# Optimization experiments

Measured on AMD Instinct MI355X. Metric: run time of the kernel, lower is better.

## Reference

```python
import jax, jax.numpy as jnp
import numpy as np

N = 50000
EH = 500000
ES = 250000
D_IN = 128
D_HID = 128
N_CLS = 47


def _mean_agg(feat, src, dst, n):
    # gather src features, scatter-mean onto dst (DGL copy_u + mean)
    msg = feat[src]                                   # [E, d]
    s = jax.ops.segment_sum(msg, dst, num_segments=n)  # [N, d]
    cnt = jax.ops.segment_sum(jnp.ones((src.shape[0],), feat.dtype), dst, num_segments=n)
    return s / jnp.maximum(cnt, 1.0)[:, None]


def _sage_cv_layer(H, HBar, W, b, hs, hd, ss, sd):
    hbar_new = _mean_agg(HBar, hs, hd, N)             # history etype
    hdelta_new = _mean_agg(H - HBar, ss, sd, N)       # sampled etype
    h_neigh = hbar_new + hdelta_new
    z = jnp.concatenate([H, h_neigh], axis=1)         # [N, 2*d_in]
    return jax.nn.relu(z @ W.T + b)


def setup_inputs() -> dict:
    key = jax.random.key(0)
    ks = jax.random.split(key, 16)
    gain = float(np.sqrt(2.0))  # calculate_gain('relu')

    def xavier(k, shape):
        fan_out, fan_in = shape
        a = gain * np.sqrt(6.0 / (fan_in + fan_out))
        return jax.random.uniform(k, shape, jnp.float32, -a, a)

    return {
        "x": jax.random.normal(ks[0], (N, D_IN), jnp.float32),
        "hbar0": jax.random.normal(ks[1], (N, D_IN), jnp.float32),
        "hbar1": jax.random.normal(ks[2], (N, D_HID), jnp.float32),
        "W0": xavier(ks[3], (D_HID, 2 * D_IN)),
        "b0": jnp.zeros((D_HID,), jnp.float32),
        "W1": xavier(ks[4], (N_CLS, 2 * D_HID)),
        "b1": jnp.zeros((N_CLS,), jnp.float32),
        "hist_src0": jax.random.randint(ks[5], (EH,), 0, N),
        "hist_dst0": jax.random.randint(ks[6], (EH,), 0, N),
        "samp_src0": jax.random.randint(ks[7], (ES,), 0, N),
        "samp_dst0": jax.random.randint(ks[8], (ES,), 0, N),
        "hist_src1": jax.random.randint(ks[9], (EH,), 0, N),
        "hist_dst1": jax.random.randint(ks[10], (EH,), 0, N),
        "samp_src1": jax.random.randint(ks[11], (ES,), 0, N),
        "samp_dst1": jax.random.randint(ks[12], (ES,), 0, N),
    }


def reference(x, hbar0, hbar1, W0, b0, W1, b1,
              hist_src0, hist_dst0, samp_src0, samp_dst0,
              hist_src1, hist_dst1, samp_src1, samp_dst1):
    h = _sage_cv_layer(x, hbar0, W0, b0, hist_src0, hist_dst0, samp_src0, samp_dst0)
    h = _sage_cv_layer(h, hbar1, W1, b1, hist_src1, hist_dst1, samp_src1, samp_dst1)
    return h  # [N, n_classes]
```

## Files before the change

kernel.cpp:

```cpp
#include <hip/hip_runtime.h>

#define D_FEAT 128
#define K_DIM  256
#define EPB 4096

typedef __attribute__((ext_vector_type(8))) short bf16x8;
typedef __attribute__((ext_vector_type(4))) float f32x4;

__device__ __forceinline__ unsigned short f2b(float f) {
    union { float f; unsigned u; } cv; cv.f = f;
    return (unsigned short)((cv.u + 0x7fffu + ((cv.u >> 16) & 1u)) >> 16);
}

__device__ __forceinline__ unsigned pack2(float lo, float hi) {
    return (unsigned)f2b(lo) | ((unsigned)f2b(hi) << 16);
}

__device__ __forceinline__ uint4 pack8(float4 a, float4 b) {
    return make_uint4(pack2(a.x, a.y), pack2(a.z, a.w), pack2(b.x, b.y), pack2(b.z, b.w));
}

__device__ __forceinline__ void addu4(float* a, uint4 v) {
    union { unsigned u; float f; } c;
    c.u = v.x << 16;         a[0] += c.f;
    c.u = v.x & 0xffff0000u; a[1] += c.f;
    c.u = v.y << 16;         a[2] += c.f;
    c.u = v.y & 0xffff0000u; a[3] += c.f;
    c.u = v.z << 16;         a[4] += c.f;
    c.u = v.z & 0xffff0000u; a[5] += c.f;
    c.u = v.w << 16;         a[6] += c.f;
    c.u = v.w & 0xffff0000u; a[7] += c.f;
}

__device__ __forceinline__ long yoff(int y, int EH, int ES) {
    return (long)((y + 1) >> 1) * EH + (long)(y >> 1) * ES;
}


__global__ __launch_bounds__(256)
void histB(const int* __restrict__ hd0, const int* __restrict__ sd0,
           const int* __restrict__ hd1, const int* __restrict__ sd1,
           int EH, int ES, int* __restrict__ bucketCnt, int nb2) {
    int y = blockIdx.y;
    const int* d = (y == 0) ? hd0 : (y == 1) ? sd0 : (y == 2) ? hd1 : sd1;
    int E = (y & 1) ? ES : EH;
    __shared__ int cnt[256];
    int t = threadIdx.x;
    cnt[t] = 0;
    __syncthreads();
    int i0 = blockIdx.x * EPB;
    #pragma unroll
    for (int j = 0; j < 16; ++j) {
        int i = i0 + j * 256 + t;
        if (i < E) atomicAdd(&cnt[d[i] >> 8], 1);
    }
    __syncthreads();
    if (t < nb2 && cnt[t] > 0) atomicAdd(&bucketCnt[y * nb2 + t], cnt[t]);
}

__global__ __launch_bounds__(64)
void scanBuckets(const int* __restrict__ bucketCnt, int* __restrict__ rpBucket,
                 int* __restrict__ bcur, int nb2) {
    int t = threadIdx.x;
    if (t < 4) {
        int run = 0;
        for (int i = 0; i < nb2; ++i) {
            rpBucket[t * (nb2 + 1) + i] = run;
            bcur[t * nb2 + i] = run;
            run += bucketCnt[t * nb2 + i];
        }
        rpBucket[t * (nb2 + 1) + nb2] = run;
    }
}

__global__ __launch_bounds__(256)
void binA(const int* __restrict__ hs0, const int* __restrict__ hd0,
          const int* __restrict__ ss0, const int* __restrict__ sd0,
          const int* __restrict__ hs1, const int* __restrict__ hd1,
          const int* __restrict__ ss1, const int* __restrict__ sd1,
          int EH, int ES, int* __restrict__ bcur, unsigned* __restrict__ recs,
          int nb2) {
    int y = blockIdx.y;
    const int* src = (y == 0) ? hs0 : (y == 1) ? ss0 : (y == 2) ? hs1 : ss1;
    const int* dst = (y == 0) ? hd0 : (y == 1) ? sd0 : (y == 2) ? hd1 : sd1;
    int E = (y & 1) ? ES : EH;
    unsigned* rb = recs + yoff(y, EH, ES);

    __shared__ int cnt[256];
    int t = threadIdx.x;
    cnt[t] = 0;
    __syncthreads();
    int i0 = blockIdx.x * EPB;
    #pragma unroll
    for (int j = 0; j < 16; ++j) {
        int i = i0 + j * 256 + t;
        if (i < E) atomicAdd(&cnt[dst[i] >> 8], 1);
    }
    __syncthreads();
    int c = cnt[t];
    __syncthreads();
    if (t < nb2 && c > 0) cnt[t] = atomicAdd(&bcur[y * nb2 + t], c);
    __syncthreads();
    #pragma unroll
    for (int j = 0; j < 16; ++j) {
        int i = i0 + j * 256 + t;
        if (i < E) {
            int dd = dst[i];
            int slot = atomicAdd(&cnt[dd >> 8], 1);
            rb[slot] = (unsigned)src[i] | ((unsigned)(dd & 255) << 24);
        }
    }
}

__global__ __launch_bounds__(256)
void placeB(const unsigned* __restrict__ recs, const int* __restrict__ rpBucket,
            int* __restrict__ rpAll, int* __restrict__ srcAll,
            int EH, int ES, int n, int nb2) {
    int y = blockIdx.y;
    int b = blockIdx.x;
    int E = (y & 1) ? ES : EH;
    int* rp = rpAll + (size_t)y * (n + 1);
    long off = yoff(y, EH, ES);
    const unsigned* rb = recs + off;
    int* sb = srcAll + off;
    int e0 = rpBucket[y * (nb2 + 1) + b];
    int e1 = rpBucket[y * (nb2 + 1) + b + 1];
    int nodeBase = b << 8;

    __shared__ int cnt[256];
    __shared__ int sh[256];
    int t = threadIdx.x;
    cnt[t] = 0;
    __syncthreads();
    for (int e = e0 + t; e < e1; e += 256)
        atomicAdd(&cnt[rb[e] >> 24], 1);
    __syncthreads();
    sh[t] = cnt[t];
    __syncthreads();
    for (int o = 1; o < 256; o <<= 1) {
        int x = (t >= o) ? sh[t - o] : 0;
        __syncthreads();
        sh[t] += x;
        __syncthreads();
    }
    int base = e0 + (t ? sh[t - 1] : 0);
    if (nodeBase + t < n) rp[nodeBase + t] = base;
    if (b == 0 && t == 0) rp[n] = E;
    cnt[t] = base;
    __syncthreads();
    for (int e = e0 + t; e < e1; e += 256) {
        unsigned r = rb[e];
        int p = atomicAdd(&cnt[r >> 24], 1);
        sb[p] = (int)(r & 0x00FFFFFFu);
    }
}

__global__ __launch_bounds__(256)
void prep_static(const float4* __restrict__ x, const float4* __restrict__ hbar0,
                 const float4* __restrict__ hbar1,
                 uint4* __restrict__ hb0, uint4* __restrict__ db0,
                 uint4* __restrict__ hb1, uint4* __restrict__ z, int n16) {
    int i = blockIdx.x * 256 + threadIdx.x;
    if (i >= n16) return;
    float4 xa = x[i * 2],     xb = x[i * 2 + 1];
    float4 ba = hbar0[i * 2], bb = hbar0[i * 2 + 1];
    float4 ca = hbar1[i * 2], cb = hbar1[i * 2 + 1];
    hb0[i] = pack8(ba, bb);
    db0[i] = pack8(make_float4(xa.x - ba.x, xa.y - ba.y, xa.z - ba.z, xa.w - ba.w),
                   make_float4(xb.x - bb.x, xb.y - bb.y, xb.z - bb.z, xb.w - bb.w));
    hb1[i] = pack8(ca, cb);
    int g = i >> 4, seg = i & 15;
    z[(size_t)g * 32 + seg] = pack8(xa, xb);
}

__global__ __launch_bounds__(256)
void conv_weights(const float* __restrict__ W0, unsigned short* __restrict__ Wb0,
                  const float* __restrict__ W1, unsigned short* __restrict__ Wb1) {
    int i = blockIdx.x * 256 + threadIdx.x;
    if (i < 128 * 256) Wb0[i] = f2b(W0[i]);
    if (i < 64 * 256) {
        int r = i >> 8;
        Wb1[i] = (r < 47) ? f2b(W1[i]) : (unsigned short)0;
    }
}

__global__ __launch_bounds__(256)
void aggregate_z(const uint4* __restrict__ HB, const uint4* __restrict__ DB,
                 const int* __restrict__ rpH, const int* __restrict__ srcH,
                 const int* __restrict__ rpS, const int* __restrict__ srcS,
                 uint4* __restrict__ z, int n) {
    int g = blockIdx.x * 4 + (threadIdx.x >> 6);
    if (g >= n) return;
    int lane = threadIdx.x & 63;
    int j = lane >> 4, l = lane & 15;

    int hb_ = rpH[g], he = rpH[g + 1];
    int sb  = rpS[g], se = rpS[g + 1];

    float a[8] = {0, 0, 0, 0, 0, 0, 0, 0};
    for (int e0 = hb_; e0 < he; e0 += 8) {
        int e1 = e0 + j, e2 = e0 + 4 + j;
        uint4 v1 = make_uint4(0, 0, 0, 0), v2 = make_uint4(0, 0, 0, 0);
        if (e1 < he) v1 = HB[(size_t)srcH[e1] * 16 + l];
        if (e2 < he) v2 = HB[(size_t)srcH[e2] * 16 + l];
        addu4(a, v1); addu4(a, v2);
    }
    float d[8] = {0, 0, 0, 0, 0, 0, 0, 0};
    for (int e0 = sb; e0 < se; e0 += 8) {
        int e1 = e0 + j, e2 = e0 + 4 + j;
        uint4 v1 = make_uint4(0, 0, 0, 0), v2 = make_uint4(0, 0, 0, 0);
        if (e1 < se) v1 = DB[(size_t)srcS[e1] * 16 + l];
        if (e2 < se) v2 = DB[(size_t)srcS[e2] * 16 + l];
        addu4(d, v1); addu4(d, v2);
    }

    float rH = 1.0f / fmaxf((float)(he - hb_), 1.0f);
    float rS = 1.0f / fmaxf((float)(se - sb), 1.0f);
    float s[8];
    #pragma unroll
    for (int i = 0; i < 8; ++i) {
        float v = a[i] * rH + d[i] * rS;
        v += __shfl_xor(v, 16);
        v += __shfl_xor(v, 32);
        s[i] = v;
    }
    if (j == 0) {
        uint4 rv = make_uint4(pack2(s[0], s[1]), pack2(s[2], s[3]),
                              pack2(s[4], s[5]), pack2(s[6], s[7]));
        z[(size_t)g * 32 + 16 + l] = rv;
    }
}

__global__ __launch_bounds__(256)
void gemm_mfma_l0(const unsigned short* __restrict__ Z, const unsigned short* __restrict__ Wb,
                  const float* __restrict__ bias, const float* __restrict__ hbar1,
                  unsigned short* __restrict__ db1, unsigned short* __restrict__ zl, int n) {
    int wave = threadIdx.x >> 6;
    int lane = threadIdx.x & 63;
    int m0 = blockIdx.x * 64 + wave * 16;
    int mr = m0 + (lane & 15);
    int mc = (mr < n) ? mr : (n - 1);
    int kq = lane >> 4;

    f32x4 acc[8] = {};
    const short* Zs = (const short*)Z;
    const short* Ws = (const short*)Wb;

    #pragma unroll
    for (int k0 = 0; k0 < 8; ++k0) {
        int ko = k0 * 32 + kq * 8;
        bf16x8 aF = *(const bf16x8*)(Zs + (size_t)mc * 256 + ko);
        #pragma unroll
        for (int t = 0; t < 8; ++t) {
            bf16x8 bF = *(const bf16x8*)(Ws + (size_t)(t * 16 + (lane & 15)) * 256 + ko);
            acc[t] = __builtin_amdgcn_mfma_f32_16x16x32_bf16(aF, bF, acc[t], 0, 0, 0);
        }
    }

    int cl = lane & 15;
    int rg = (lane >> 4) * 4;
    #pragma unroll
    for (int r = 0; r < 4; ++r) {
        int m = m0 + rg + r;
        if (m >= n) continue;
        #pragma unroll
        for (int t = 0; t < 8; ++t) {
            int c = t * 16 + cl;
            float h = fmaxf(acc[t][r] + bias[c], 0.0f);
            float hbv = hbar1[(size_t)m * 128 + c];
            db1[(size_t)m * 128 + c] = f2b(h - hbv);
            zl[(size_t)m * 256 + c]  = f2b(h);
        }
    }
}

template<int NT>
__global__ __launch_bounds__(256)
void gemm_mfma(const unsigned short* __restrict__ Z, const unsigned short* __restrict__ Wb,
               const float* __restrict__ bias, float* __restrict__ out, int n, int COLS) {
    int wave = threadIdx.x >> 6;
    int lane = threadIdx.x & 63;
    int m0 = blockIdx.x * 64 + wave * 16;
    int mr = m0 + (lane & 15);
    int mc = (mr < n) ? mr : (n - 1);
    int kq = lane >> 4;

    f32x4 acc[NT] = {};
    const short* Zs = (const short*)Z;
    const short* Ws = (const short*)Wb;

    #pragma unroll
    for (int k0 = 0; k0 < 8; ++k0) {
        int ko = k0 * 32 + kq * 8;
        bf16x8 aF = *(const bf16x8*)(Zs + (size_t)mc * 256 + ko);
        #pragma unroll
        for (int t = 0; t < NT; ++t) {
            bf16x8 bF = *(const bf16x8*)(Ws + (size_t)(t * 16 + (lane & 15)) * 256 + ko);
            acc[t] = __builtin_amdgcn_mfma_f32_16x16x32_bf16(aF, bF, acc[t], 0, 0, 0);
        }
    }

    int cl = lane & 15;
    int rg = (lane >> 4) * 4;
    #pragma unroll
    for (int t = 0; t < NT; ++t) {
        int c = t * 16 + cl;
        if (c >= COLS) continue;
        float bv = bias[c];
        #pragma unroll
        for (int r = 0; r < 4; ++r) {
            int m = m0 + rg + r;
            if (m < n) out[(size_t)m * COLS + c] = fmaxf(acc[t][r] + bv, 0.f);
        }
    }
}

extern "C" void kernel_launch(void* const* d_in, const int* in_sizes, int n_in,
                              void* d_out, int out_size, void* d_ws, size_t ws_size,
                              hipStream_t stream) {
    const float* x     = (const float*)d_in[0];
    const float* hbar0 = (const float*)d_in[1];
    const float* hbar1 = (const float*)d_in[2];
    const float* W0    = (const float*)d_in[3];
    const float* b0    = (const float*)d_in[4];
    const float* W1    = (const float*)d_in[5];
    const float* b1    = (const float*)d_in[6];
    const int* hs0 = (const int*)d_in[7];
    const int* hd0 = (const int*)d_in[8];
    const int* ss0 = (const int*)d_in[9];
    const int* sd0 = (const int*)d_in[10];
    const int* hs1 = (const int*)d_in[11];
    const int* hd1 = (const int*)d_in[12];
    const int* ss1 = (const int*)d_in[13];
    const int* sd1 = (const int*)d_in[14];

    const int n   = in_sizes[0] / D_FEAT;
    const int EH  = in_sizes[7];
    const int ES  = in_sizes[9];
    const int nb2 = (n + 255) / 256;

    int* bucketCnt = (int*)d_ws;
    int* rpBucket  = bucketCnt + 4 * nb2;
    int* bcur      = rpBucket + 4 * (nb2 + 1);
    int* rpAll     = bcur + 4 * nb2;
    int* srcAll    = rpAll + 4 * (size_t)(n + 1);
    unsigned* recs = (unsigned*)(srcAll + 2 * (size_t)EH + 2 * (size_t)ES);
    size_t int_words = (size_t)12 * nb2 + 4 + 4 * (size_t)(n + 1)
                     + 4 * (size_t)EH + 4 * (size_t)ES;
    int_words = (int_words + 3) & ~(size_t)3;
    unsigned short* hb0 = (unsigned short*)((int*)d_ws + int_words);
    unsigned short* db0 = hb0 + (size_t)n * D_FEAT;
    unsigned short* hb1 = db0 + (size_t)n * D_FEAT;
    unsigned short* db1 = hb1 + (size_t)n * D_FEAT;
    unsigned short* z   = db1 + (size_t)n * D_FEAT;
    unsigned short* Wb0 = z + (size_t)n * K_DIM;
    unsigned short* Wb1 = Wb0 + 128 * 256;

    const int* rpH0 = rpAll;
    const int* rpS0 = rpAll + (size_t)(n + 1);
    const int* rpH1 = rpAll + 2 * (size_t)(n + 1);
    const int* rpS1 = rpAll + 3 * (size_t)(n + 1);
    int* srcH0 = srcAll;
    int* srcS0 = srcAll + (size_t)EH;
    int* srcH1 = srcAll + (size_t)EH + ES;
    int* srcS1 = srcAll + 2 * (size_t)EH + ES;

    dim3 blk(256);
    int binb  = (EH + EPB - 1) / EPB;
    int prepb = ((n * 16) + 255) / 256;
    int aggb  = (n + 3) / 4;
    int gemmb = (n + 63) / 64;

    hipMemsetAsync(bucketCnt, 0, 4 * (size_t)nb2 * sizeof(int), stream);
    conv_weights<<<128, blk, 0, stream>>>(W0, Wb0, W1, Wb1);
    histB<<<dim3(binb, 4), blk, 0, stream>>>(hd0, sd0, hd1, sd1, EH, ES, bucketCnt, nb2);
    scanBuckets<<<1, 64, 0, stream>>>(bucketCnt, rpBucket, bcur, nb2);
    binA<<<dim3(binb, 4), blk, 0, stream>>>(hs0, hd0, ss0, sd0, hs1, hd1, ss1, sd1,
                                            EH, ES, bcur, recs, nb2);
    placeB<<<dim3(nb2, 4), blk, 0, stream>>>(recs, rpBucket, rpAll, srcAll, EH, ES, n, nb2);
    prep_static<<<prepb, blk, 0, stream>>>((const float4*)x, (const float4*)hbar0,
                                           (const float4*)hbar1, (uint4*)hb0, (uint4*)db0,
                                           (uint4*)hb1, (uint4*)z, n * 16);

    aggregate_z<<<aggb, blk, 0, stream>>>((const uint4*)hb0, (const uint4*)db0,
                                          rpH0, srcH0, rpS0, srcS0, (uint4*)z, n);
    gemm_mfma_l0<<<gemmb, blk, 0, stream>>>(z, Wb0, b0, hbar1, db1, z, n);

    aggregate_z<<<aggb, blk, 0, stream>>>((const uint4*)hb1, (const uint4*)db1,
                                          rpH1, srcH1, rpS1, srcS1, (uint4*)z, n);
    gemm_mfma<3><<<gemmb, blk, 0, stream>>>(z, Wb1, b1, (float*)d_out, n, 47);
}
```

Baseline: 344.4 us.

## Stage layer-0 GEMM epilogue through LDS, double-buffer fragment loads, shrink tiles

The layer-0 GEMM now splits each 32-row tile across four waves, two row tiles by two column halves, and writes the ReLU output to padded LDS. It then re-reads that output as rows to do coalesced 16-byte stores of z and db1 and vectorised float4 reads of hbar1, replacing scattered 2-byte stores. Both GEMMs double-buffer their A/B fragment loads across k-steps to overlap loads with MFMAs. The layer-1 GEMM uses 128-thread blocks covering 32 rows for more blocks. This costs extra LDS, a sync and more registers for the prefetch buffers.

Result: no change. 341.4 us (-0.9%).

```diff
diff --git a/kernel.cpp b/kernel.cpp
--- a/kernel.cpp
+++ b/kernel.cpp
@@ -3,6 +3,7 @@
 #define D_FEAT 128
 #define K_DIM  256
 #define EPB 4096
+#define PADL 136
 
 typedef __attribute__((ext_vector_type(8))) short bf16x8;
 typedef __attribute__((ext_vector_type(4))) float f32x4;
@@ -31,6 +32,9 @@
     c.u = v.w << 16;         a[6] += c.f;
     c.u = v.w & 0xffff0000u; a[7] += c.f;
 }
+
+__device__ __forceinline__ float blo(unsigned u) { union { unsigned u; float f; } c; c.u = u << 16; return c.f; }
+__device__ __forceinline__ float bhi(unsigned u) { union { unsigned u; float f; } c; c.u = u & 0xffff0000u; return c.f; }
 
 __device__ __forceinline__ long yoff(int y, int EH, int ES) {
     return (long)((y + 1) >> 1) * EH + (long)(y >> 1) * ES;
@@ -235,73 +239,125 @@
 void gemm_mfma_l0(const unsigned short* __restrict__ Z, const unsigned short* __restrict__ Wb,
                   const float* __restrict__ bias, const float* __restrict__ hbar1,
                   unsigned short* __restrict__ db1, unsigned short* __restrict__ zl, int n) {
-    int wave = threadIdx.x >> 6;
-    int lane = threadIdx.x & 63;
-    int m0 = blockIdx.x * 64 + wave * 16;
-    int mr = m0 + (lane & 15);
+    __shared__ unsigned short hl[32 * PADL];
+    int tid  = threadIdx.x;
+    int wave = tid >> 6;
+    int lane = tid & 63;
+    int rt = wave >> 1;
+    int ch = wave & 1;
+    int m0 = blockIdx.x * 32;
+    int cl = lane & 15;
+    int kq = lane >> 4;
+
+    int mr = m0 + rt * 16 + cl;
     int mc = (mr < n) ? mr : (n - 1);
-    int kq = lane >> 4;
-
-    f32x4 acc[8] = {};
+
     const short* Zs = (const short*)Z;
     const short* Ws = (const short*)Wb;
+    const short* aP = Zs + (size_t)mc * 256 + kq * 8;
+    const short* bP = Ws + (size_t)(ch * 64 + cl) * 256 + kq * 8;
+
+    f32x4 acc[4] = {};
+    bf16x8 aF[2];
+    bf16x8 bF[2][4];
+    aF[0] = *(const bf16x8*)(aP);
+    #pragma unroll
+    for (int t = 0; t < 4; ++t) bF[0][t] = *(const bf16x8*)(bP + t * 16 * 256);
 
     #pragma unroll
     for (int k0 = 0; k0 < 8; ++k0) {
-        int ko = k0 * 32 + kq * 8;
-        bf16x8 aF = *(const bf16x8*)(Zs + (size_t)mc * 256 + ko);
+        int cur = k0 & 1, nxt = cur ^ 1;
+        if (k0 < 7) {
+            int ko = (k0 + 1) * 32;
+            aF[nxt] = *(const bf16x8*)(aP + ko);
+            #pragma unroll
+            for (int t = 0; t < 4; ++t)
+                bF[nxt][t] = *(const bf16x8*)(bP + t * 16 * 256 + ko);
+        }
         #pragma unroll
-        for (int t = 0; t < 8; ++t) {
-            bf16x8 bF = *(const bf16x8*)(Ws + (size_t)(t * 16 + (lane & 15)) * 256 + ko);
-            acc[t] = __builtin_amdgcn_mfma_f32_16x16x32_bf16(aF, bF, acc[t], 0, 0, 0);
-        }
-    }
-
-    int cl = lane & 15;
-    int rg = (lane >> 4) * 4;
-    #pragma unroll
-    for (int r = 0; r < 4; ++r) {
-        int m = m0 + rg + r;
-        if (m >= n) continue;
+        for (int t = 0; t < 4; ++t)
+            acc[t] = __builtin_amdgcn_mfma_f32_16x16x32_bf16(aF[cur], bF[cur][t], acc[t], 0, 0, 0);
+    }
+
+    #pragma unroll
+    for (int t = 0; t < 4; ++t) {
+        int c = ch * 64 + t * 16 + cl;
+        float bv = bias[c];
         #pragma unroll
-        for (int t = 0; t < 8; ++t) {
-            int c = t * 16 + cl;
-            float h = fmaxf(acc[t][r] + bias[c], 0.0f);
-            float hbv = hbar1[(size_t)m * 128 + c];
-            db1[(size_t)m * 128 + c] = f2b(h - hbv);
-            zl[(size_t)m * 256 + c]  = f2b(h);
-        }
+        for (int r = 0; r < 4; ++r) {
+            int row = rt * 16 + kq * 4 + r;
+            hl[row * PADL + c] = f2b(fmaxf(acc[t][r] + bv, 0.0f));
+        }
+    }
+    __syncthreads();
+
+    int row  = tid >> 3;
+    int col  = (tid & 7) * 16;
+    int m    = m0 + row;
+    if (m < n) {
+        const uint4* hr = (const uint4*)(hl + row * PADL + col);
+        uint4 v0 = hr[0];
+        uint4 v1 = hr[1];
+        uint4* zp = (uint4*)(zl + (size_t)m * 256 + col);
+        zp[0] = v0;
+        zp[1] = v1;
+        const float4* hb = (const float4*)(hbar1 + (size_t)m * 128 + col);
+        float4 h0 = hb[0], h1 = hb[1], h2 = hb[2], h3 = hb[3];
+        uint4 d0, d1;
+        d0.x = pack2(blo(v0.x) - h0.x, bhi(v0.x) - h0.y);
+        d0.y = pack2(blo(v0.y) - h0.z, bhi(v0.y) - h0.w);
+        d0.z = pack2(blo(v0.z) - h1.x, bhi(v0.z) - h1.y);
+        d0.w = pack2(blo(v0.w) - h1.z, bhi(v0.w) - h1.w);
+        d1.x = pack2(blo(v1.x) - h2.x, bhi(v1.x) - h2.y);
+        d1.y = pack2(blo(v1.y) - h2.z, bhi(v1.y) - h2.w);
+        d1.z = pack2(blo(v1.z) - h3.x, bhi(v1.z) - h3.y);
+        d1.w = pack2(blo(v1.w) - h3.z, bhi(v1.w) - h3.w);
+        uint4* dp = (uint4*)(db1 + (size_t)m * 128 + col);
+        dp[0] = d0;
+        dp[1] = d1;
     }
 }
 
 template<int NT>
-__global__ __launch_bounds__(256)
+__global__ __launch_bounds__(128)
 void gemm_mfma(const unsigned short* __restrict__ Z, const unsigned short* __restrict__ Wb,
                const float* __restrict__ bias, float* __restrict__ out, int n, int COLS) {
     int wave = threadIdx.x >> 6;
     int lane = threadIdx.x & 63;
-    int m0 = blockIdx.x * 64 + wave * 16;
+    int m0 = blockIdx.x * 32 + wave * 16;
     int mr = m0 + (lane & 15);
     int mc = (mr < n) ? mr : (n - 1);
     int kq = lane >> 4;
-
-    f32x4 acc[NT] = {};
+    int cl = lane & 15;
+
     const short* Zs = (const short*)Z;
     const short* Ws = (const short*)Wb;
+    const short* aP = Zs + (size_t)mc * 256 + kq * 8;
+    const short* bP = Ws + (size_t)cl * 256 + kq * 8;
+
+    f32x4 acc[NT] = {};
+    bf16x8 aF[2];
+    bf16x8 bF[2][NT];
+    aF[0] = *(const bf16x8*)(aP);
+    #pragma unroll
+    for (int t = 0; t < NT; ++t) bF[0][t] = *(const bf16x8*)(bP + t * 16 * 256);
 
     #pragma unroll
     for (int k0 = 0; k0 < 8; ++k0) {
-        int ko = k0 * 32 + kq * 8;
-        bf16x8 aF = *(const bf16x8*)(Zs + (size_t)mc * 256 + ko);
+        int cur = k0 & 1, nxt = cur ^ 1;
+        if (k0 < 7) {
+            int ko = (k0 + 1) * 32;
+            aF[nxt] = *(const bf16x8*)(aP + ko);
+            #pragma unroll
+            for (int t = 0; t < NT; ++t)
+                bF[nxt][t] = *(const bf16x8*)(bP + t * 16 * 256 + ko);
+        }
         #pragma unroll
-        for (int t = 0; t < NT; ++t) {
-            bf16x8 bF = *(const bf16x8*)(Ws + (size_t)(t * 16 + (lane & 15)) * 256 + ko);
-            acc[t] = __builtin_amdgcn_mfma_f32_16x16x32_bf16(aF, bF, acc[t], 0, 0, 0);
-        }
-    }
-
-    int cl = lane & 15;
-    int rg = (lane >> 4) * 4;
+        for (int t = 0; t < NT; ++t)
+            acc[t] = __builtin_amdgcn_mfma_f32_16x16x32_bf16(aF[cur], bF[cur][t], acc[t], 0, 0, 0);
+    }
+
+    int rg = kq * 4;
     #pragma unroll
     for (int t = 0; t < NT; ++t) {
         int c = t * 16 + cl;
@@ -369,7 +425,8 @@
     int binb  = (EH + EPB - 1) / EPB;
     int prepb = ((n * 16) + 255) / 256;
     int aggb  = (n + 3) / 4;
-    int gemmb = (n + 63) / 64;
+    int gemmb0 = (n + 31) / 32;
+    int gemmb1 = (n + 31) / 32;
 
     hipMemsetAsync(bucketCnt, 0, 4 * (size_t)nb2 * sizeof(int), stream);
     conv_weights<<<128, blk, 0, stream>>>(W0, Wb0, W1, Wb1);
@@ -384,9 +441,9 @@
 
     aggregate_z<<<aggb, blk, 0, stream>>>((const uint4*)hb0, (const uint4*)db0,
                                           rpH0, srcH0, rpS0, srcS0, (uint4*)z, n);
-    gemm_mfma_l0<<<gemmb, blk, 0, stream>>>(z, Wb0, b0, hbar1, db1, z, n);
+    gemm_mfma_l0<<<gemmb0, blk, 0, stream>>>(z, Wb0, b0, hbar1, db1, z, n);
 
     aggregate_z<<<aggb, blk, 0, stream>>>((const uint4*)hb1, (const uint4*)db1,
                                           rpH1, srcH1, rpS1, srcS1, (uint4*)z, n);
-    gemm_mfma<3><<<gemmb, blk, 0, stream>>>(z, Wb1, b1, (float*)d_out, n, 47);
-}
+    gemm_mfma<3><<<gemmb1, dim3(128), 0, stream>>>(z, Wb1, b1, (float*)d_out, n, 47);
+}
```
